# Performance work log

Measured on AMD Instinct MI355X. Metric: run time of the kernel, lower is better.

Reference implementation:

```python
import jax, jax.numpy as jnp
import numpy as np
from jax import lax

T, B, I, H = 2048, 64, 256, 256  # seq_len, batch, input_size, hidden_size


def setup_inputs() -> dict:
    key = jax.random.key(0)
    k1, k2, k3, k4 = jax.random.split(key, 4)
    scale = 1.0 / np.sqrt(H)  # ~ torch Linear default init magnitude
    x = jax.random.normal(k1, (T, B, I), dtype=jnp.float32)
    w_in = jax.random.normal(k2, (4 * H, I), dtype=jnp.float32) * scale
    b = jax.random.normal(k3, (4 * H,), dtype=jnp.float32) * scale
    w_rec = jax.random.normal(k4, (4 * H, H), dtype=jnp.float32) * scale
    return {"x": x, "w_in": w_in, "b": b, "w_rec": w_rec}


def reference(x, w_in, b, w_rec):
    # x: [T, B, I] (batch_first=False). Single-layer vanilla subLSTM.
    # Precompute input projection for all timesteps (one big GEMM).
    gx = jnp.einsum('tbi,gi->tbg', x, w_in) + b  # [T, B, 4H]
    h0 = jnp.zeros((x.shape[1], w_rec.shape[1]), dtype=x.dtype)
    c0 = jnp.zeros_like(h0)

    def cell(carry, gxt):
        h, c = carry
        gates = jax.nn.sigmoid(gxt + h @ w_rec.T)  # all 4 gates sigmoid
        i_g, o_g, z_g, f_g = jnp.split(gates, 4, axis=-1)
        c_new = f_g * c + z_g - i_g          # subtractive input gate
        h_new = jax.nn.sigmoid(c_new) - o_g  # subtractive output gate
        return (h_new, c_new), h_new

    (h_last, c_last), outputs = lax.scan(cell, (h0, c0), gx)
    return outputs  # [T, B, H]
```

## Files before the change

### kernel.cpp

```cpp
#include <hip/hip_runtime.h>
#include <cstdint>
#include <cstddef>

typedef __attribute__((ext_vector_type(8))) short short8;
typedef __attribute__((ext_vector_type(4))) float f32x4;
typedef __attribute__((ext_vector_type(4))) unsigned int u32x4;
typedef __attribute__((ext_vector_type(4))) int i32x4;

#define NEG_LOG2E -1.44269504088896340736f
#define MFMA_BF16 __builtin_amdgcn_mfma_f32_16x16x32_bf16
#define MFMA_I8 __builtin_amdgcn_mfma_i32_16x16x64_i8

static __device__ __forceinline__ unsigned int cvt_pk_bf16(float lo, float hi) {
  unsigned int r;
  asm("v_cvt_pk_bf16_f32 %0, %1, %2" : "=v"(r) : "v"(lo), "v"(hi));
  return r;
}
static __device__ __forceinline__ float sigmoid_scaled(float xs) {
  return __builtin_amdgcn_rcpf(1.0f + __builtin_amdgcn_exp2f(xs));
}

__global__ void wscale_setup(const float* __restrict__ w_rec,
                             float* __restrict__ scbuf,
                             float* __restrict__ w127) {
  const int j = blockIdx.x;
  const int l = threadIdx.x;
  const float* row = w_rec + (size_t)j * 256;
  float m = 0.f;
#pragma unroll
  for (int k = 0; k < 4; ++k) m = fmaxf(m, fabsf(row[l + 64 * k]));
#pragma unroll
  for (int d = 32; d > 0; d >>= 1) m = fmaxf(m, __shfl_xor(m, d));
  if (l == 0) {
    float s = fmaxf(m * 1.44269504088896f, 1e-30f);
    scbuf[j] = s / 16129.0f;
    w127[j] = 127.0f / s;
  }
}

__global__ void wfrag_setup_i8(const float* __restrict__ w_rec,
                               const float* __restrict__ w127,
                               unsigned int* __restrict__ wfq) {
  const int f = blockIdx.x;
  const int l = threadIdx.x;
  const int w = f >> 6, q = f & 63;
  const int chain = q >> 2, kt = q & 3;
  const int jidx = chain >> 2, g = chain & 3;
  const int jt = (jidx < 2) ? (2 * w + jidx) : (2 * w + 8 + (jidx - 2));
  const int ct = jt + 16 * g;
  const int j = ct * 16 + (l & 15);
  const float r = w127[j];
  const float* src = w_rec + (size_t)j * 256 + kt * 64 + (l >> 4) * 16;
  u32x4 ov;
#pragma unroll
  for (int d = 0; d < 4; ++d) {
    unsigned int word = 0;
#pragma unroll
    for (int e = 0; e < 4; ++e) {
      int qi = (int)rintf(src[4 * d + e] * NEG_LOG2E * r);
      qi = qi > 127 ? 127 : (qi < -127 ? -127 : qi);
      word |= ((unsigned int)(qi & 255)) << (8 * e);
    }
    ov[d] = word;
  }
  *(u32x4*)(wfq + (size_t)f * 256 + (size_t)l * 4) = ov;
}

static __device__ __forceinline__ short8 ldcvt8(const float* p) {
  f32x4 v0 = *(const f32x4*)p;
  f32x4 v1 = *(const f32x4*)(p + 4);
  u32x4 u;
  u[0] = cvt_pk_bf16(v0[0], v0[1]);
  u[1] = cvt_pk_bf16(v0[2], v0[3]);
  u[2] = cvt_pk_bf16(v1[0], v1[1]);
  u[3] = cvt_pk_bf16(v1[2], v1[3]);
  return __builtin_bit_cast(short8, u);
}

__global__ __launch_bounds__(256) void gemm_gx(const float* __restrict__ x,
                                               const float* __restrict__ w_in,
                                               const float* __restrict__ bias,
                                               unsigned int* __restrict__ gx) {
  const int n = blockIdx.x;
  const int bx = (n >> 3) & 7;
  const int by = (n >> 6) * 8 + (n & 7);
  const int l = threadIdx.x & 63, wid = threadIdx.x >> 6;
  const int mq = wid >> 1, nq = wid & 1;
  const int mbase = by * 128 + mq * 64;
  const int nbase = bx * 128 + nq * 64;
  const int lr = l & 15;
  const int lk = (l >> 4) * 8;

  f32x4 acc[4][4] = {};
#pragma unroll
  for (int kt = 0; kt < 8; ++kt) {
    const int k0 = kt * 32 + lk;
    short8 af[4], bf[4];
#pragma unroll
    for (int mt = 0; mt < 4; ++mt)
      af[mt] = ldcvt8(x + (size_t)(mbase + mt * 16 + lr) * 256 + k0);
#pragma unroll
    for (int nt = 0; nt < 4; ++nt)
      bf[nt] = ldcvt8(w_in + (size_t)(nbase + nt * 16 + lr) * 256 + k0);
#pragma unroll
    for (int mt = 0; mt < 4; ++mt)
#pragma unroll
      for (int nt = 0; nt < 4; ++nt)
        acc[mt][nt] = MFMA_BF16(af[mt], bf[nt], acc[mt][nt], 0, 0, 0);
  }

  float bv[4];
#pragma unroll
  for (int nt = 0; nt < 4; ++nt) bv[nt] = bias[nbase + nt * 16 + lr];

#pragma unroll
  for (int mt = 0; mt < 4; ++mt) {
    const int m0 = mbase + mt * 16;
    const int tt = m0 >> 6;
    const int bg = ((m0 & 63) >> 2) + (l >> 4);
#pragma unroll
    for (int ntp = 0; ntp < 2; ++ntp) {
      const int p = (nbase >> 5) + ntp;
      const int pb = p & 7, g = p >> 3;
#pragma unroll
      for (int r = 0; r < 4; ++r) {
        float e0 = (acc[mt][ntp * 2 + 0][r] + bv[ntp * 2 + 0]) * NEG_LOG2E;
        float e1 = (acc[mt][ntp * 2 + 1][r] + bv[ntp * 2 + 1]) * NEG_LOG2E;
        gx[(((((size_t)tt * 16 + bg) * 8 + pb) * 64) + (r * 16 + lr)) * 4 + g] =
            cvt_pk_bf16(e0, e1);
      }
    }
  }
}

#define HB8_ROW 288
#define HB8_SZ (4 * HB8_ROW)
#define LDS_TOTAL (2 * HB8_SZ)

#define LD4A(i)                                                         \
  asm volatile("global_load_dwordx4 %0, %4, off\n\t"                    \
               "global_load_dwordx4 %1, %4, off offset:1024\n\t"        \
               "global_load_dwordx4 %2, %4, off offset:2048\n\t"        \
               "global_load_dwordx4 %3, %4, off offset:3072"            \
               : "=&a"(wa[4 * (i)]), "=&a"(wa[4 * (i) + 1]),            \
                 "=&a"(wa[4 * (i) + 2]), "=&a"(wa[4 * (i) + 3])         \
               : "v"(pA + 4096 * (i)))

__global__ __launch_bounds__(1024) void rnn_scan(
    const unsigned int* __restrict__ wfq, const float* __restrict__ scbuf,
    const unsigned int* __restrict__ gx, float* __restrict__ out,
    float* __restrict__ hstate, float* __restrict__ cstate, int first) {
  extern __shared__ char lds[];
  char* hb0 = lds;
  char* hb1 = lds + HB8_SZ;

  const int l = threadIdx.x & 63;
  const int w = threadIdx.x >> 6;
  const int bg = blockIdx.x;
  const int bloc = l >> 4;
  const int col = l & 15;
  const int jt = w;
  const int fbase = (jt < 8) ? ((jt >> 1) * 64 + (jt & 1) * 16)
                             : (((jt - 8) >> 1) * 64 + (2 + (jt & 1)) * 16);

  i32x4 wa[16];
  {
    const char* pA = (const char*)wfq + (size_t)fbase * 1024 + (size_t)l * 16;
    LD4A(0); LD4A(1); LD4A(2); LD4A(3);
    asm volatile("s_waitcnt vmcnt(0)" ::: "memory");
  }
  float scv[4];
#pragma unroll
  for (int g = 0; g < 4; ++g)
    scv[g] = scbuf[(jt + 16 * g) * 16 + col];

  float carr;
  if (first) {
    for (int i = threadIdx.x; i < (2 * HB8_SZ) / 4; i += 1024)
      ((unsigned int*)hb0)[i] = 0u;
    carr = 0.0f;
  } else {
    const size_t idx = (size_t)(bg * 4 + bloc) * 256 + jt * 16 + col;
    carr = cstate[idx];
    const int qi = (int)rintf(hstate[idx] * 127.f);
    *(char*)(hb0 + bloc * HB8_ROW + jt * 16 + col) = (char)qi;
  }

  u32x4 gxA, gxB;
  {
    const unsigned int* g0 =
        gx + ((((size_t)0 * 16 + bg) * 8 + (jt >> 1)) << 8) + 4 * l;
    gxA = *(const u32x4*)g0;
  }
  __syncthreads();

  float* outp = out + (size_t)(bg * 4 + bloc) * 256 + col + jt * 16;
  const int aoff = ((l & 15) >> 2) * HB8_ROW + (l >> 4) * 16;
  const int hwoff = bloc * HB8_ROW;
  const bool hi = (jt & 1) != 0;

  auto STEP = [&](int t, char* hbR, char* hbW, u32x4& gxC, u32x4& gxN) {
    const int tn = (t + 1 < 512) ? (t + 1) : 511;
    const unsigned int* gn =
        gx + ((((size_t)tn * 16 + bg) * 8 + (jt >> 1)) << 8) + 4 * l;
    gxN = *(const u32x4*)gn;

    const char* hrd = hbR + aoff;
    i32x4 afv[4];
#pragma unroll
    for (int kt = 0; kt < 4; ++kt)
      afv[kt] = *(const i32x4*)(hrd + kt * 64);

    i32x4 d0 = {0, 0, 0, 0}, d1 = d0, d2 = d0, d3 = d0;
#pragma unroll
    for (int kt = 0; kt < 4; ++kt) {
      d0 = MFMA_I8(afv[kt], wa[kt], d0, 0, 0, 0);
      d1 = MFMA_I8(afv[kt], wa[4 + kt], d1, 0, 0, 0);
      d2 = MFMA_I8(afv[kt], wa[8 + kt], d2, 0, 0, 0);
      d3 = MFMA_I8(afv[kt], wa[12 + kt], d3, 0, 0, 0);
    }

    {
      const float g0f = hi ? __uint_as_float(gxC[0] & 0xffff0000u)
                           : __uint_as_float(gxC[0] << 16);
      const float g1f = hi ? __uint_as_float(gxC[1] & 0xffff0000u)
                           : __uint_as_float(gxC[1] << 16);
      const float g2f = hi ? __uint_as_float(gxC[2] & 0xffff0000u)
                           : __uint_as_float(gxC[2] << 16);
      const float g3f = hi ? __uint_as_float(gxC[3] & 0xffff0000u)
                           : __uint_as_float(gxC[3] << 16);
      const float gi = sigmoid_scaled(fmaf((float)d0[0], scv[0], g0f));
      const float go = sigmoid_scaled(fmaf((float)d1[0], scv[1], g1f));
      const float gz = sigmoid_scaled(fmaf((float)d2[0], scv[2], g2f));
      const float gf = sigmoid_scaled(fmaf((float)d3[0], scv[3], g3f));
      carr = gf * carr + (gz - gi);
      const float hs = sigmoid_scaled(carr * NEG_LOG2E);
      const float hn = hs - go;
      outp[(size_t)t * 16384] = hn;
      const int qh = (int)rintf(hn * 127.f);
      *(char*)(hbW + hwoff + jt * 16 + col) = (char)qh;
    }

    __builtin_amdgcn_sched_barrier(0);
    asm volatile("s_waitcnt lgkmcnt(0)");
    __builtin_amdgcn_s_barrier();
    __builtin_amdgcn_sched_barrier(0);
  };

  for (int tt = 0; tt < 256; ++tt) {
    STEP(2 * tt, hb0, hb1, gxA, gxB);
    STEP(2 * tt + 1, hb1, hb0, gxB, gxA);
  }

  {
    const size_t idx = (size_t)(bg * 4 + bloc) * 256 + jt * 16 + col;
    const signed char qv =
        *(const signed char*)(hb0 + hwoff + jt * 16 + col);
    hstate[idx] = (float)qv / 127.f;
    cstate[idx] = carr;
  }
}

extern "C" void kernel_launch(void* const* d_in, const int* in_sizes, int n_in,
                              void* d_out, int out_size, void* d_ws,
                              size_t ws_size, hipStream_t stream) {
  const float* x = (const float*)d_in[0];
  const float* w_in = (const float*)d_in[1];
  const float* bias = (const float*)d_in[2];
  const float* wrec = (const float*)d_in[3];
  float* out = (float*)d_out;
  char* ws = (char*)d_ws;

  unsigned int* wfq = (unsigned int*)ws;
  float* scbuf = (float*)(ws + (256 << 10));
  float* w127 = (float*)(ws + (260 << 10));
  float* hstate = (float*)(ws + (512 << 10));
  float* cstate = (float*)(ws + (576 << 10));
  unsigned int* gxb = (unsigned int*)(ws + (1 << 20));

  (void)in_sizes; (void)n_in; (void)out_size; (void)ws_size;

  wscale_setup<<<dim3(1024), dim3(64), 0, stream>>>(wrec, scbuf, w127);
  wfrag_setup_i8<<<dim3(256), dim3(64), 0, stream>>>(wrec, w127, wfq);

  for (int c = 0; c < 4; ++c) {
    const size_t xoff = (size_t)c * 512 * 64 * 256;
    gemm_gx<<<dim3(2048), dim3(256), 0, stream>>>(x + xoff, w_in, bias, gxb);
    rnn_scan<<<dim3(16), dim3(1024), LDS_TOTAL, stream>>>(
        wfq, scbuf, gxb, out + xoff, hstate, cstate, (c == 0) ? 1 : 0);
  }
}
```

Measured before the change: 2.122 ms.

## Overlap next chunk's input GEMM with recurrent scan in one fused launch

Adds extra blocks to the scan kernel that compute the input projection for the next time chunk into a second, double-buffered gx buffer while the 16 scan blocks process the current chunk. The chunk length drops from 512 to 256 steps, giving 8 launches instead of 4 with separate GEMM launches. This is meant to hide the GEMM cost behind the latency-bound serial scan, which leaves most CUs idle. The risk is that the GEMM blocks contend with the scan blocks for memory bandwidth and may slow the critical path. The GEMM MFMA chain uses hand-written asm with manual s_nop hazard padding.

Result: faster. 1.720 ms (-18.9%).

```diff
diff --git a/kernel.cpp b/kernel.cpp
--- a/kernel.cpp
+++ b/kernel.cpp
@@ -10,6 +10,7 @@
 #define NEG_LOG2E -1.44269504088896340736f
 #define MFMA_BF16 __builtin_amdgcn_mfma_f32_16x16x32_bf16
 #define MFMA_I8 __builtin_amdgcn_mfma_i32_16x16x64_i8
+#define CH 256
 
 static __device__ __forceinline__ unsigned int cvt_pk_bf16(float lo, float hi) {
   unsigned int r;
@@ -19,6 +20,31 @@
 static __device__ __forceinline__ float sigmoid_scaled(float xs) {
   return __builtin_amdgcn_rcpf(1.0f + __builtin_amdgcn_exp2f(xs));
 }
+
+#define GMF8_BODY                                        \
+  "v_mfma_f32_16x16x32_bf16 %0, %8, %12, %0\n\t"         \
+  "v_mfma_f32_16x16x32_bf16 %1, %8, %13, %1\n\t"         \
+  "v_mfma_f32_16x16x32_bf16 %2, %9, %12, %2\n\t"         \
+  "v_mfma_f32_16x16x32_bf16 %3, %9, %13, %3\n\t"         \
+  "v_mfma_f32_16x16x32_bf16 %4, %10, %12, %4\n\t"        \
+  "v_mfma_f32_16x16x32_bf16 %5, %10, %13, %5\n\t"        \
+  "v_mfma_f32_16x16x32_bf16 %6, %11, %12, %6\n\t"        \
+  "v_mfma_f32_16x16x32_bf16 %7, %11, %13, %7"
+#define GMF8_OUTS                                                          \
+  "+&a"(c00), "+&a"(c01), "+&a"(c10), "+&a"(c11), "+&a"(c20), "+&a"(c21),  \
+  "+&a"(c30), "+&a"(c31)
+#define GMF8_INS                                                           \
+  "v"(a0), "v"(a1), "v"(a2), "v"(a3), "v"(b0), "v"(b1)
+#define DEF_GMF8(name, lead, tail)                                         \
+  static __device__ __forceinline__ void name(                             \
+      short8 a0, short8 a1, short8 a2, short8 a3, short8 b0, short8 b1,    \
+      f32x4& c00, f32x4& c01, f32x4& c10, f32x4& c11, f32x4& c20,          \
+      f32x4& c21, f32x4& c30, f32x4& c31) {                                \
+    asm(lead GMF8_BODY tail : GMF8_OUTS : GMF8_INS);                       \
+  }
+DEF_GMF8(gmf8_first, "s_nop 3\n\t", "")
+DEF_GMF8(gmf8_mid, "", "")
+DEF_GMF8(gmf8_last, "", "\n\ts_nop 7\n\ts_nop 7\n\ts_nop 3")
 
 __global__ void wscale_setup(const float* __restrict__ w_rec,
                              float* __restrict__ scbuf,
@@ -146,10 +172,67 @@
                  "=&a"(wa[4 * (i) + 2]), "=&a"(wa[4 * (i) + 3])         \
                : "v"(pA + 4096 * (i)))
 
-__global__ __launch_bounds__(1024) void rnn_scan(
+__global__ __launch_bounds__(1024) void scan_gemm(
     const unsigned int* __restrict__ wfq, const float* __restrict__ scbuf,
     const unsigned int* __restrict__ gx, float* __restrict__ out,
-    float* __restrict__ hstate, float* __restrict__ cstate, int first) {
+    float* __restrict__ hstate, float* __restrict__ cstate, int first,
+    const float* __restrict__ xn, const float* __restrict__ w_in,
+    const float* __restrict__ bias, unsigned int* __restrict__ gxn,
+    int do_gemm) {
+  if (blockIdx.x >= 16) {
+    if (!do_gemm) return;
+    const int mm = blockIdx.x - 16;
+    const int by = mm >> 2;
+    const int sub = threadIdx.x >> 8;
+    const int strip = ((mm & 3) << 2) + sub;
+    const int tix = threadIdx.x & 255;
+    const int l = tix & 63, wid = tix >> 6;
+    const int mq = wid >> 1, nq = wid & 1;
+    const int mbase = by * 128 + mq * 64;
+    const int nbase = strip * 64 + nq * 32;
+    const int lr = l & 15, lk = (l >> 4) * 8;
+
+    f32x4 c00 = {0.f, 0.f, 0.f, 0.f}, c01 = c00, c10 = c00, c11 = c00;
+    f32x4 c20 = c00, c21 = c00, c30 = c00, c31 = c00;
+#pragma unroll
+    for (int kt = 0; kt < 8; ++kt) {
+      const int k0 = kt * 32 + lk;
+      const short8 a0 = ldcvt8(xn + (size_t)(mbase + 0 * 16 + lr) * 256 + k0);
+      const short8 a1 = ldcvt8(xn + (size_t)(mbase + 1 * 16 + lr) * 256 + k0);
+      const short8 a2 = ldcvt8(xn + (size_t)(mbase + 2 * 16 + lr) * 256 + k0);
+      const short8 a3 = ldcvt8(xn + (size_t)(mbase + 3 * 16 + lr) * 256 + k0);
+      const short8 b0 = ldcvt8(w_in + (size_t)(nbase + 0 * 16 + lr) * 256 + k0);
+      const short8 b1 = ldcvt8(w_in + (size_t)(nbase + 1 * 16 + lr) * 256 + k0);
+      if (kt == 0)
+        gmf8_first(a0, a1, a2, a3, b0, b1, c00, c01, c10, c11, c20, c21, c30, c31);
+      else if (kt < 7)
+        gmf8_mid(a0, a1, a2, a3, b0, b1, c00, c01, c10, c11, c20, c21, c30, c31);
+      else
+        gmf8_last(a0, a1, a2, a3, b0, b1, c00, c01, c10, c11, c20, c21, c30, c31);
+    }
+
+    const float bv0 = bias[nbase + lr];
+    const float bv1 = bias[nbase + 16 + lr];
+    const int p = nbase >> 5;
+    const int pb = p & 7, g = p >> 3;
+    const f32x4* accm[4][2] = {{&c00, &c01}, {&c10, &c11},
+                               {&c20, &c21}, {&c30, &c31}};
+#pragma unroll
+    for (int mt = 0; mt < 4; ++mt) {
+      const int m0 = mbase + mt * 16;
+      const int tt = m0 >> 6;
+      const int bg = ((m0 & 63) >> 2) + (l >> 4);
+#pragma unroll
+      for (int r = 0; r < 4; ++r) {
+        float e0 = ((*accm[mt][0])[r] + bv0) * NEG_LOG2E;
+        float e1 = ((*accm[mt][1])[r] + bv1) * NEG_LOG2E;
+        gxn[(((((size_t)tt * 16 + bg) * 8 + pb) * 64) + (r * 16 + lr)) * 4 + g] =
+            cvt_pk_bf16(e0, e1);
+      }
+    }
+    return;
+  }
+
   extern __shared__ char lds[];
   char* hb0 = lds;
   char* hb1 = lds + HB8_SZ;
@@ -200,7 +283,7 @@
   const bool hi = (jt & 1) != 0;
 
   auto STEP = [&](int t, char* hbR, char* hbW, u32x4& gxC, u32x4& gxN) {
-    const int tn = (t + 1 < 512) ? (t + 1) : 511;
+    const int tn = (t + 1 < CH) ? (t + 1) : (CH - 1);
     const unsigned int* gn =
         gx + ((((size_t)tn * 16 + bg) * 8 + (jt >> 1)) << 8) + 4 * l;
     gxN = *(const u32x4*)gn;
@@ -247,7 +330,7 @@
     __builtin_amdgcn_sched_barrier(0);
   };
 
-  for (int tt = 0; tt < 256; ++tt) {
+  for (int tt = 0; tt < CH / 2; ++tt) {
     STEP(2 * tt, hb0, hb1, gxA, gxB);
     STEP(2 * tt + 1, hb1, hb0, gxB, gxA);
   }
@@ -276,17 +359,22 @@
   float* w127 = (float*)(ws + (260 << 10));
   float* hstate = (float*)(ws + (512 << 10));
   float* cstate = (float*)(ws + (576 << 10));
-  unsigned int* gxb = (unsigned int*)(ws + (1 << 20));
+  unsigned int* gxb[2] = {(unsigned int*)(ws + (1ull << 20)),
+                          (unsigned int*)(ws + (33ull << 20))};
 
   (void)in_sizes; (void)n_in; (void)out_size; (void)ws_size;
 
   wscale_setup<<<dim3(1024), dim3(64), 0, stream>>>(wrec, scbuf, w127);
   wfrag_setup_i8<<<dim3(256), dim3(64), 0, stream>>>(wrec, w127, wfq);
 
-  for (int c = 0; c < 4; ++c) {
-    const size_t xoff = (size_t)c * 512 * 64 * 256;
-    gemm_gx<<<dim3(2048), dim3(256), 0, stream>>>(x + xoff, w_in, bias, gxb);
-    rnn_scan<<<dim3(16), dim3(1024), LDS_TOTAL, stream>>>(
-        wfq, scbuf, gxb, out + xoff, hstate, cstate, (c == 0) ? 1 : 0);
-  }
-}
+  const size_t chelt = (size_t)CH * 64 * 256;
+  gemm_gx<<<dim3(1024), dim3(256), 0, stream>>>(x, w_in, bias, gxb[0]);
+
+  for (int c = 0; c < 8; ++c) {
+    const int nxt = (c + 1 < 8) ? (c + 1) : 0;
+    scan_gemm<<<dim3(16 + 512), dim3(1024), LDS_TOTAL, stream>>>(
+        wfq, scbuf, gxb[c & 1], out + (size_t)c * chelt, hstate, cstate,
+        (c == 0) ? 1 : 0, x + (size_t)nxt * chelt, w_in, bias,
+        gxb[(c + 1) & 1], (c < 7) ? 1 : 0);
+  }
+}
```
